# Kernel tuning notes

Hardware: AMD Instinct MI355X
Metric: run time of the kernel (lower is better)

## Reference

```python
import jax, jax.numpy as jnp
import numpy as np

B, C, L, E = 32, 3, 512, 512


def setup_inputs() -> dict:
    key = jax.random.key(0)
    ks = jax.random.split(key, 13)
    bnd = float(np.sqrt(6.0 / (2.0 * E)))  # xavier-uniform-like bound
    uni = lambda k, shp: jax.random.uniform(k, shp, jnp.float32, -bnd, bnd)
    return {
        "A0": jax.random.normal(ks[0], (B, C, L, L), jnp.float32),
        "x0": jax.random.normal(ks[1], (B, C, L, E), jnp.float32),
        "u0": jax.random.normal(ks[2], (B, C, E), jnp.float32),
        "t0": jax.random.normal(ks[3], (B, E), jnp.float32),
        "t1": jax.random.normal(ks[4], (B, E), jnp.float32),
        "Q_weight": uni(ks[5], (C, E, E)),
        "Q_bias": jnp.zeros((C, E), jnp.float32),
        "V_weight": uni(ks[6], (C, E, E)),
        "V_bias": jnp.zeros((C, E), jnp.float32),
        "K_weight": uni(ks[7], (C, E, E)),
        "K_bias": jnp.zeros((C, E), jnp.float32),
        "T_weight": uni(ks[8], (C, E, E)),
        "T_bias": jnp.zeros((C, E), jnp.float32),
    }


def reference(A0, x0, u0, t0, t1,
              Q_weight, Q_bias, V_weight, V_bias,
              K_weight, K_bias, T_weight, T_bias):
    # Time embeddings: (B,E) @ (C,E,E) -> (B,C,E)
    T0 = jnp.einsum('be,cef->bcf', t0, T_weight)
    T1 = jnp.einsum('be,cef->bcf', t1, T_weight)

    # Original modulates weight columns: x @ (W * T) == (x @ W) * T (T broadcasts
    # over the input axis via unsqueeze(-2)); use the fused, equivalent form.
    Q = jnp.einsum('bce,cef->bcf', x0[:, :, -1, :], Q_weight) * T0 + Q_bias  # (B,C,E)
    K = jnp.einsum('bce,cef->bcf', u0, K_weight) * T1 + K_bias               # (B,C,E)
    V = jnp.einsum('bcle,cef->bclf', x0, V_weight) * T1[:, :, None, :] \
        + V_bias[None, :, None, :]                                           # (B,C,L,E)

    QKV = jax.nn.softmax(jnp.einsum('bce,bcle->bcl', Q * K, V), axis=-1)     # (B,C,L)

    # A1[:, :, i, :] = A0[:, :, i+1, :] - A0[:, :, 0, :] for i < L-1;
    # A1[:, :, L-1, :] = A1[:, :, L-2, :] + QKV  (= A0[-1] - A0[0] + QKV)
    rows = A0[:, :, 1:, :] - A0[:, :, :1, :]                                 # (B,C,L-1,L)
    last = rows[:, :, -1, :] + QKV                                           # (B,C,L)
    A1 = jnp.concatenate([rows, last[:, :, None, :]], axis=2)                # (B,C,L,L)

    x1 = jnp.einsum('bclm,bcme->bcle', A1, x0)                               # (B,C,L,E)
    x1 = jnp.diff(x1, axis=2, prepend=jnp.zeros_like(x1[:, :, :1, :]))

    num = jnp.sum(T0 * T1, axis=-1)                                          # (B,C)
    den = jnp.sqrt(jnp.sum(T0 * T0, axis=-1) + jnp.sum(T1 * T1, axis=-1))
    w = (num / den)[..., None]                                               # (B,C,1)

    u1 = u0 * (1.0 - w) + x1.mean(axis=-2) * w                               # (B,C,E)
    return (A1 - A0, x1 - x0, u1 - u0)
```

## Files before the change

kernel.cpp:

```cpp
#include <hip/hip_runtime.h>
#include <stdint.h>

#define BB 32
#define CC 3
#define LL 512
#define EE 512
#define NBC (BB*CC)

#define O2_OFF ((size_t)NBC*LL*LL)
#define O3_OFF (O2_OFF + (size_t)NBC*LL*EE)

#define WSB_QX    0
#define WSB_H     196608
#define WSB_W     442368
#define WSB_ADIFF ((size_t)512*1024)
#define ADIFF_BYTES ((size_t)NBC*LL*LL*2)
#define WSB_X0T   (WSB_ADIFF + ADIFF_BYTES)
#define WS_FAST_NEED (WSB_X0T + ADIFF_BYTES)

#define NEC 16

typedef short bf16x8 __attribute__((ext_vector_type(8)));
typedef float f32x4  __attribute__((ext_vector_type(4)));

__device__ __forceinline__ float wred_sum(float v){
#pragma unroll
  for (int m = 32; m >= 1; m >>= 1) v += __shfl_xor(v, m, 64);
  return v;
}
__device__ __forceinline__ float wred_max(float v){
#pragma unroll
  for (int m = 32; m >= 1; m >>= 1) v = fmaxf(v, __shfl_xor(v, m, 64));
  return v;
}
__device__ __forceinline__ void f4ma(float4& a, float s, const float4& b){
  a.x = fmaf(s, b.x, a.x); a.y = fmaf(s, b.y, a.y);
  a.z = fmaf(s, b.z, a.z); a.w = fmaf(s, b.w, a.w);
}
__device__ __forceinline__ float4 f4sub(const float4& a, const float4& b){
  return make_float4(a.x-b.x, a.y-b.y, a.z-b.z, a.w-b.w);
}
__device__ __forceinline__ unsigned short f2bf(float x){
  unsigned u = __float_as_uint(x);
  return (unsigned short)((u + 0x7FFFu + ((u >> 16) & 1u)) >> 16);
}
__device__ __forceinline__ float bf2f(unsigned short h){
  return __uint_as_float(((unsigned)h) << 16);
}
__device__ __forceinline__ void split1(float v, unsigned short& hi, unsigned short& lo){
  hi = f2bf(v);
  lo = f2bf(v - bf2f(hi));
}

__global__ __launch_bounds__(512) void k0p(
    const float* __restrict__ x0, const float* __restrict__ u0,
    const float* __restrict__ t0, const float* __restrict__ t1,
    const float* __restrict__ Qw, const float* __restrict__ Kw,
    const float* __restrict__ Tw,
    float* __restrict__ P)
{
  const int bg = blockIdx.x;
  const int c  = blockIdx.y;
  const int ec = blockIdx.z;
  const int b0 = bg*4;
  const int e0 = ec*32;
  const int f  = threadIdx.x;
  __shared__ float vb[4][4][32];
  {
    int vec = f >> 7, j = (f >> 5) & 3, e = f & 31;
    int bb = b0 + j;
    float v;
    if      (vec == 0) v = t0[bb*EE + e0 + e];
    else if (vec == 1) v = t1[bb*EE + e0 + e];
    else if (vec == 2) v = x0[((size_t)(bb*CC + c)*LL + (LL-1))*EE + e0 + e];
    else               v = u0[(size_t)(bb*CC + c)*EE + e0 + e];
    vb[vec][j][e] = v;
  }
  __syncthreads();

  const float* twp = Tw + (size_t)c*EE*EE + (size_t)e0*EE + f;
  const float* qwp = Qw + (size_t)c*EE*EE + (size_t)e0*EE + f;
  const float* kwp = Kw + (size_t)c*EE*EE + (size_t)e0*EE + f;
  float aT0[4]={0,0,0,0}, aT1[4]={0,0,0,0}, aQ[4]={0,0,0,0}, aK[4]={0,0,0,0};
#pragma unroll 8
  for (int e = 0; e < 32; ++e) {
    float wt = twp[(size_t)e*EE];
    float wq = qwp[(size_t)e*EE];
    float wk = kwp[(size_t)e*EE];
#pragma unroll
    for (int j = 0; j < 4; ++j) {
      aT0[j] = fmaf(vb[0][j][e], wt, aT0[j]);
      aT1[j] = fmaf(vb[1][j][e], wt, aT1[j]);
      aQ[j]  = fmaf(vb[2][j][e], wq, aQ[j]);
      aK[j]  = fmaf(vb[3][j][e], wk, aK[j]);
    }
  }
#pragma unroll
  for (int j = 0; j < 4; ++j) {
    int cb = c*BB + b0 + j;
    P[(((size_t)0*NEC + ec)*96 + cb)*EE + f] = aT0[j];
    P[(((size_t)1*NEC + ec)*96 + cb)*EE + f] = aT1[j];
    P[(((size_t)2*NEC + ec)*96 + cb)*EE + f] = aQ[j];
    P[(((size_t)3*NEC + ec)*96 + cb)*EE + f] = aK[j];
  }
}

__global__ __launch_bounds__(512) void k0c(
    const float* __restrict__ P,
    const float* __restrict__ Qb, const float* __restrict__ Kb,
    float* __restrict__ gtbuf, float* __restrict__ ws_w)
{
  const int bc = blockIdx.x;
  const int b = bc / CC, c = bc % CC;
  const int cb = c*BB + b;
  const int f = threadIdx.x;
  const int wid = f >> 6, lane = f & 63;
  __shared__ float red[8][3];
  float aT0=0.f, aT1=0.f, aQ=0.f, aK=0.f;
#pragma unroll
  for (int ec = 0; ec < NEC; ++ec) {
    aT0 += P[(((size_t)0*NEC + ec)*96 + cb)*EE + f];
    aT1 += P[(((size_t)1*NEC + ec)*96 + cb)*EE + f];
    aQ  += P[(((size_t)2*NEC + ec)*96 + cb)*EE + f];
    aK  += P[(((size_t)3*NEC + ec)*96 + cb)*EE + f];
  }
  float Qv = aQ*aT0 + Qb[c*EE + f];
  float Kv = aK*aT1 + Kb[c*EE + f];
  gtbuf[(size_t)cb*EE + f] = Qv*Kv*aT1;
  float pn = wred_sum(aT0*aT1);
  float p0 = wred_sum(aT0*aT0);
  float p1 = wred_sum(aT1*aT1);
  if (lane == 0) { red[wid][0]=pn; red[wid][1]=p0; red[wid][2]=p1; }
  __syncthreads();
  if (f == 0) {
    float sn=0.f, s0=0.f, s1=0.f;
    for (int i=0;i<8;++i){ sn+=red[i][0]; s0+=red[i][1]; s1+=red[i][2]; }
    ws_w[bc] = sn / sqrtf(s0 + s1);
  }
}

__global__ __launch_bounds__(256) void k1_h(
    const float* __restrict__ Vw, const float* __restrict__ gtbuf,
    float* __restrict__ ws_h)
{
  const int nt = blockIdx.x;
  const int c  = blockIdx.y;
  const int n0 = nt*128;
  const int t = threadIdx.x, lane = t & 63, w = t >> 6;
  __shared__ __align__(16) char AgtH[32*1024];
  __shared__ __align__(16) char AgtL[32*1024];
  __shared__ __align__(16) char BvH[128*128];
  __shared__ __align__(16) char BvL[128*128];
  {
    int row = t >> 3, sl = t & 7;
    const float* src = gtbuf + ((size_t)(c*BB + row))*EE + sl*64;
#pragma unroll
    for (int c3 = 0; c3 < 8; ++c3) {
      float4 a = *reinterpret_cast<const float4*>(src + c3*8);
      float4 b = *reinterpret_cast<const float4*>(src + c3*8 + 4);
      ushort4 h0,h1,l0,l1;
      split1(a.x,h0.x,l0.x); split1(a.y,h0.y,l0.y); split1(a.z,h0.z,l0.z); split1(a.w,h0.w,l0.w);
      split1(b.x,h1.x,l1.x); split1(b.y,h1.y,l1.y); split1(b.z,h1.z,l1.z); split1(b.w,h1.w,l1.w);
      int off = row*1024 + sl*128 + ((c3 ^ (row & 7)) << 4);
      *reinterpret_cast<ushort4*>(AgtH + off)     = h0;
      *reinterpret_cast<ushort4*>(AgtH + off + 8) = h1;
      *reinterpret_cast<ushort4*>(AgtL + off)     = l0;
      *reinterpret_cast<ushort4*>(AgtL + off + 8) = l1;
    }
  }
  f32x4 acc[2][2];
#pragma unroll
  for (int mi=0; mi<2; ++mi)
#pragma unroll
    for (int ni=0; ni<2; ++ni) acc[mi][ni] = (f32x4){0.f,0.f,0.f,0.f};

  for (int kk = 0; kk < 8; ++kk) {
    __syncthreads();
    {
      int nl = t >> 1, half = t & 1;
      const float* src = Vw + (size_t)c*EE*EE + (size_t)(n0+nl)*EE + kk*64 + half*32;
#pragma unroll
      for (int q = 0; q < 4; ++q) {
        float4 a = *reinterpret_cast<const float4*>(src + q*8);
        float4 b = *reinterpret_cast<const float4*>(src + q*8 + 4);
        int c3 = half*4 + q;
        ushort4 h0,h1,l0,l1;
        split1(a.x,h0.x,l0.x); split1(a.y,h0.y,l0.y); split1(a.z,h0.z,l0.z); split1(a.w,h0.w,l0.w);
        split1(b.x,h1.x,l1.x); split1(b.y,h1.y,l1.y); split1(b.z,h1.z,l1.z); split1(b.w,h1.w,l1.w);
        int off = nl*128 + ((c3 ^ (nl & 7)) << 4);
        *reinterpret_cast<ushort4*>(BvH + off)     = h0;
        *reinterpret_cast<ushort4*>(BvH + off + 8) = h1;
        *reinterpret_cast<ushort4*>(BvL + off)     = l0;
        *reinterpret_cast<ushort4*>(BvL + off + 8) = l1;
      }
    }
    __syncthreads();
    bf16x8 afH[2][2], afL[2][2], bfH[2][2], bfL[2][2];
#pragma unroll
    for (int mi=0; mi<2; ++mi)
#pragma unroll
      for (int ks=0; ks<2; ++ks) {
        int row = mi*16 + (lane & 15);
        int c3 = ks*4 + (lane >> 4);
        int off = row*1024 + kk*128 + ((c3 ^ (row & 7)) << 4);
        afH[mi][ks] = *reinterpret_cast<const bf16x8*>(AgtH + off);
        afL[mi][ks] = *reinterpret_cast<const bf16x8*>(AgtL + off);
      }
#pragma unroll
    for (int ni=0; ni<2; ++ni)
#pragma unroll
      for (int ks=0; ks<2; ++ks) {
        int n = w*32 + ni*16 + (lane & 15);
        int c3 = ks*4 + (lane >> 4);
        int off = n*128 + ((c3 ^ (n & 7)) << 4);
        bfH[ni][ks] = *reinterpret_cast<const bf16x8*>(BvH + off);
        bfL[ni][ks] = *reinterpret_cast<const bf16x8*>(BvL + off);
      }
#pragma unroll
    for (int mi=0; mi<2; ++mi)
#pragma unroll
      for (int ni=0; ni<2; ++ni)
#pragma unroll
        for (int ks=0; ks<2; ++ks) {
          acc[mi][ni] = __builtin_amdgcn_mfma_f32_16x16x32_bf16(afH[mi][ks], bfH[ni][ks], acc[mi][ni], 0, 0, 0);
          acc[mi][ni] = __builtin_amdgcn_mfma_f32_16x16x32_bf16(afH[mi][ks], bfL[ni][ks], acc[mi][ni], 0, 0, 0);
          acc[mi][ni] = __builtin_amdgcn_mfma_f32_16x16x32_bf16(afL[mi][ks], bfH[ni][ks], acc[mi][ni], 0, 0, 0);
        }
  }
#pragma unroll
  for (int mi=0; mi<2; ++mi)
#pragma unroll
    for (int ni=0; ni<2; ++ni)
#pragma unroll
      for (int r=0; r<4; ++r) {
        int b = mi*16 + (lane >> 4)*4 + r;
        int e = n0 + w*32 + ni*16 + (lane & 15);
        ws_h[((size_t)(b*CC + c))*EE + e] = acc[mi][ni][r];
      }
}

__global__ __launch_bounds__(512) void k2a_softmax(
    const float* __restrict__ A0, const float* __restrict__ x0,
    const float* __restrict__ ws_h,
    float* __restrict__ out1)
{
  const int bc = blockIdx.x;
  const int tid = threadIdx.x, wid = tid >> 6, lane = tid & 63;
  __shared__ __align__(16) float hb[EE], sb[LL], a0r0[LL];
  __shared__ float red[8];
  const size_t abase = (size_t)bc*LL*LL;
  const size_t xbase = (size_t)bc*LL*EE;
  hb[tid]   = ws_h[(size_t)bc*EE + tid];
  a0r0[tid] = A0[abase + tid];
  __syncthreads();
  const float4 h0 = *reinterpret_cast<const float4*>(&hb[lane*8]);
  const float4 h1 = *reinterpret_cast<const float4*>(&hb[lane*8+4]);
  for (int l = wid; l < LL; l += 8) {
    const float4* xr = reinterpret_cast<const float4*>(x0 + xbase + (size_t)l*EE);
    float4 v0 = xr[lane*2], v1 = xr[lane*2+1];
    float acc = v0.x*h0.x + v0.y*h0.y + v0.z*h0.z + v0.w*h0.w
              + v1.x*h1.x + v1.y*h1.y + v1.z*h1.z + v1.w*h1.w;
    acc = wred_sum(acc);
    if (lane == 0) sb[l] = acc;
  }
  __syncthreads();
  float v = sb[tid];
  float mx = wred_max(v);
  if (lane == 0) red[wid] = mx;
  __syncthreads();
  mx = red[0];
#pragma unroll
  for (int i = 1; i < 8; ++i) mx = fmaxf(mx, red[i]);
  float ev = __expf(v - mx);
  float sm = wred_sum(ev);
  __syncthreads();
  if (lane == 0) red[wid] = sm;
  __syncthreads();
  float tot = 0.f;
#pragma unroll
  for (int i = 0; i < 8; ++i) tot += red[i];
  float qk = ev / tot;
  out1[abase + (size_t)(LL-1)*LL + tid] = qk - a0r0[tid];
}

__global__ __launch_bounds__(512) void k2b_cols(
    const float* __restrict__ A0, const float* __restrict__ x0,
    const float* __restrict__ u0, const float* __restrict__ out1,
    const float* __restrict__ ws_w,
    float* __restrict__ ws_qx, float* __restrict__ out3)
{
  const int bc = blockIdx.x;
  const int tid = threadIdx.x;
  const size_t abase = (size_t)bc*LL*LL;
  const size_t xbase = (size_t)bc*LL*EE;
  __shared__ __align__(16) float qkv[LL], r0v[LL], r3v[LL];
  __shared__ float partl[4][12][128];
  {
    float a0 = A0[abase + tid];
    float a3 = A0[abase + (size_t)(LL-1)*LL + tid];
    qkv[tid] = out1[abase + (size_t)(LL-1)*LL + tid] + a0;
    r0v[tid] = a0;
    r3v[tid] = a3;
  }
  __syncthreads();
  const int mg = tid >> 7, cg = tid & 127;
  float4 aq = make_float4(0,0,0,0), a0s = make_float4(0,0,0,0), a3s = make_float4(0,0,0,0);
#pragma unroll 4
  for (int i = 0; i < 128; ++i) {
    int m = mg*128 + i;
    float4 xv = *reinterpret_cast<const float4*>(x0 + xbase + (size_t)m*EE + cg*4);
    float qm = qkv[m], z0 = r0v[m], z3 = r3v[m];
    f4ma(aq, qm, xv); f4ma(a0s, z0, xv); f4ma(a3s, z3, xv);
  }
#pragma unroll
  for (int k = 0; k < 4; ++k) {
    partl[mg][0+k][cg] = (&aq.x)[k];
    partl[mg][4+k][cg] = (&a0s.x)[k];
    partl[mg][8+k][cg] = (&a3s.x)[k];
  }
  __syncthreads();
  if (mg == 0) {
    float wv = ws_w[bc];
    float4 uv = *reinterpret_cast<const float4*>(u0 + (size_t)bc*EE + cg*4);
    float4 qx4, o3;
#pragma unroll
    for (int k = 0; k < 4; ++k) {
      float q = 0.f, y0 = 0.f, y3 = 0.f;
#pragma unroll
      for (int g = 0; g < 4; ++g) {
        q  += partl[g][0+k][cg];
        y0 += partl[g][4+k][cg];
        y3 += partl[g][8+k][cg];
      }
      (&qx4.x)[k] = q;
      (&o3.x)[k] = wv * ((y3 - y0 + q) * (1.f/(float)LL) - (&uv.x)[k]);
    }
    *reinterpret_cast<float4*>(ws_qx + (size_t)bc*EE + cg*4) = qx4;
    *reinterpret_cast<float4*>(out3 + (size_t)bc*EE + cg*4) = o3;
  }
}

__global__ __launch_bounds__(512) void k_conv2(
    const float* __restrict__ A0, const float* __restrict__ x0,
    float* __restrict__ out1, char* __restrict__ adiff, char* __restrict__ x0t)
{
  const int bc = blockIdx.x;
  const int tile = blockIdx.y;
  const int t = threadIdx.x;
  if (blockIdx.z == 0) {
    const int r0 = tile*64;
    const size_t abase = (size_t)bc*LL*LL;
    char* ad = adiff + (size_t)bc*LL*LL*2;
    __shared__ __align__(16) float r0f[LL];
    r0f[t] = A0[abase + t];
    __syncthreads();
#pragma unroll 4
    for (int rep = 0; rep < 16; ++rep) {
      int pos = rep*512 + t;
      int rl = pos >> 7;
      int q  = pos & 127;
      int gr = r0 + rl;
      float4 d;
      if (gr < LL-1) {
        float4 a = *reinterpret_cast<const float4*>(A0 + abase + (size_t)gr*LL + q*4);
        float4 b = *reinterpret_cast<const float4*>(A0 + abase + (size_t)(gr+1)*LL + q*4);
        d = make_float4(b.x-a.x, b.y-a.y, b.z-a.z, b.w-a.w);
        float4 z = *reinterpret_cast<const float4*>(&r0f[q*4]);
        *reinterpret_cast<float4*>(out1 + abase + (size_t)gr*LL + q*4) = f4sub(d, z);
      } else {
        d = make_float4(0.f,0.f,0.f,0.f);
      }
      ushort4 pk;
      pk.x = f2bf(d.x); pk.y = f2bf(d.y); pk.z = f2bf(d.z); pk.w = f2bf(d.w);
      *reinterpret_cast<ushort4*>(ad + (size_t)gr*1024 + q*8) = pk;
    }
  } else {
    const int m0 = tile*64;
    const size_t xbase = (size_t)bc*LL*EE;
    char* xt = x0t + (size_t)bc*LL*EE*2;
    __shared__ float T[64][65];
    for (int ech = 0; ech < 8; ++ech) {
      const int e0 = ech*64;
      {
        int ml = t >> 3, seg = t & 7;
        const float* src = x0 + xbase + (size_t)(m0+ml)*EE + e0 + seg*8;
        float4 v0 = *reinterpret_cast<const float4*>(src);
        float4 v1 = *reinterpret_cast<const float4*>(src+4);
        T[ml][seg*8+0]=v0.x; T[ml][seg*8+1]=v0.y; T[ml][seg*8+2]=v0.z; T[ml][seg*8+3]=v0.w;
        T[ml][seg*8+4]=v1.x; T[ml][seg*8+5]=v1.y; T[ml][seg*8+6]=v1.z; T[ml][seg*8+7]=v1.w;
      }
      __syncthreads();
      {
        int el = t >> 3, c3 = t & 7;
        int eg = e0 + el;
        int mb = c3*8;
        ushort4 p0, p1;
        p0.x = f2bf(T[mb+0][el]); p0.y = f2bf(T[mb+1][el]);
        p0.z = f2bf(T[mb+2][el]); p0.w = f2bf(T[mb+3][el]);
        p1.x = f2bf(T[mb+4][el]); p1.y = f2bf(T[mb+5][el]);
        p1.z = f2bf(T[mb+6][el]); p1.w = f2bf(T[mb+7][el]);
        char* dst = xt + (size_t)eg*1024 + (size_t)(m0 + mb)*2;
        *reinterpret_cast<ushort4*>(dst) = p0;
        *reinterpret_cast<ushort4*>(dst + 8) = p1;
      }
      __syncthreads();
    }
  }
}

#define ASTR 80
__global__ __launch_bounds__(256) void k3_bf(
    const char* __restrict__ adiff, const char* __restrict__ x0t,
    const float* __restrict__ x0, const float* __restrict__ ws_qx,
    float* __restrict__ out2)
{
  const int bc = blockIdx.y;
  const int rt = blockIdx.x >> 2, nt = blockIdx.x & 3;
  const int r0 = rt*128, n0b = nt*128;
  const int t = threadIdx.x;
  const int lane = t & 63, wid = t >> 6;
  const int wr = wid >> 1, wc = wid & 1;
  __shared__ __align__(16) char As[128*ASTR];
  __shared__ __align__(16) char Bs[128*ASTR];
  const char* ad = adiff + (size_t)bc*LL*LL*2;
  const char* xt = x0t  + (size_t)bc*LL*EE*2;
  const size_t xbase = (size_t)bc*LL*EE;
  f32x4 acc[4][4];
#pragma unroll
  for (int mi=0; mi<4; ++mi)
#pragma unroll
    for (int ni=0; ni<4; ++ni) acc[mi][ni] = (f32x4){0.f,0.f,0.f,0.f};

  for (int k0 = 0; k0 < LL; k0 += 32) {
    __syncthreads();
#pragma unroll
    for (int i = 0; i < 2; ++i) {
      int idx = i*256 + t;
      int row = idx >> 2, c = idx & 3;
      int4 v = *reinterpret_cast<const int4*>(ad + (size_t)(r0+row)*1024 + k0*2 + c*16);
      *reinterpret_cast<int4*>(As + row*ASTR + c*16) = v;
    }
#pragma unroll
    for (int i = 0; i < 2; ++i) {
      int idx = i*256 + t;
      int n = idx >> 2, c = idx & 3;
      int4 v = *reinterpret_cast<const int4*>(xt + (size_t)(n0b+n)*1024 + k0*2 + c*16);
      int kb = (c*16) ^ (((n >> 2) & 3) << 4);
      *reinterpret_cast<int4*>(Bs + n*ASTR + kb) = v;
    }
    __syncthreads();
    bf16x8 af[4], bfv[4];
#pragma unroll
    for (int mi=0; mi<4; ++mi) {
      int row = wr*64 + mi*16 + (lane & 15);
      af[mi] = *reinterpret_cast<const bf16x8*>(As + row*ASTR + ((lane>>4)*16));
    }
#pragma unroll
    for (int ni=0; ni<4; ++ni) {
      int n = wc*64 + ni*16 + (lane & 15);
      int kb = ((lane>>4)*16) ^ (((n >> 2) & 3) << 4);
      bfv[ni] = *reinterpret_cast<const bf16x8*>(Bs + n*ASTR + kb);
    }
#pragma unroll
    for (int mi=0; mi<4; ++mi)
#pragma unroll
      for (int ni=0; ni<4; ++ni)
        acc[mi][ni] = __builtin_amdgcn_mfma_f32_16x16x32_bf16(af[mi], bfv[ni], acc[mi][ni], 0, 0, 0);
  }
#pragma unroll
  for (int mi=0; mi<4; ++mi)
#pragma unroll
    for (int r=0; r<4; ++r) {
      int grow = r0 + wr*64 + mi*16 + (lane>>4)*4 + r;
      const size_t rowoff = xbase + (size_t)grow*EE;
#pragma unroll
      for (int ni=0; ni<4; ++ni) {
        int gcol = n0b + wc*64 + ni*16 + (lane & 15);
        float xv = x0[rowoff + gcol];
        float val;
        if (grow == LL-1) val = ws_qx[(size_t)bc*EE + gcol] - xv;
        else              val = acc[mi][ni][r] - xv;
        out2[rowoff + gcol] = val;
      }
    }
}

__global__ __launch_bounds__(512) void kA_fused(
    const float* __restrict__ A0, const float* __restrict__ x0,
    const float* __restrict__ u0,
    const float* __restrict__ t0, const float* __restrict__ t1,
    const float* __restrict__ Qw, const float* __restrict__ Qb,
    const float* __restrict__ Vw,
    const float* __restrict__ Kw, const float* __restrict__ Kb,
    const float* __restrict__ Tw,
    float* __restrict__ ws_qx, float* __restrict__ out1, float* __restrict__ out3)
{
  const int bc = blockIdx.x;
  const int b = bc / CC, c = bc % CC;
  const int tid = threadIdx.x;
  const int wid = tid >> 6, lane = tid & 63;
  __shared__ __align__(16) float t0v[EE], t1v[EE], xl[EE], uv[EE], gt[EE];
  __shared__ __align__(16) float hb[EE], sb[LL], a0r0[LL], a0r3[LL];
  __shared__ float red[3][8];
  __shared__ float wsh;
  const size_t abase = (size_t)bc*LL*LL;
  const size_t xbase = (size_t)bc*LL*EE;

  t0v[tid] = t0[b*EE + tid];
  t1v[tid] = t1[b*EE + tid];
  xl[tid]  = x0[xbase + (size_t)(LL-1)*EE + tid];
  uv[tid]  = u0[(size_t)bc*EE + tid];
  a0r0[tid] = A0[abase + tid];
  a0r3[tid] = A0[abase + (size_t)(LL-1)*LL + tid];
  __syncthreads();

  const int f = tid;
  const float* twp = Tw + (size_t)c*EE*EE + f;
  const float* qwp = Qw + (size_t)c*EE*EE + f;
  const float* kwp = Kw + (size_t)c*EE*EE + f;
  float aT0 = 0.f, aT1 = 0.f, aQ = 0.f, aK = 0.f;
  for (int e = 0; e < EE; ++e) {
    float wt = twp[(size_t)e*EE];
    aT0 = fmaf(t0v[e], wt, aT0);
    aT1 = fmaf(t1v[e], wt, aT1);
    aQ  = fmaf(xl[e],  qwp[(size_t)e*EE], aQ);
    aK  = fmaf(uv[e],  kwp[(size_t)e*EE], aK);
  }
  float Qv = aQ*aT0 + Qb[c*EE + f];
  float Kv = aK*aT1 + Kb[c*EE + f];
  gt[f] = Qv*Kv*aT1;

  float pn = wred_sum(aT0*aT1);
  float p0 = wred_sum(aT0*aT0);
  float p1 = wred_sum(aT1*aT1);
  if (lane == 0) { red[0][wid]=pn; red[1][wid]=p0; red[2][wid]=p1; }
  __syncthreads();
  if (tid == 0) {
    float sn=0.f, s0=0.f, s1=0.f;
    for (int i=0;i<8;++i){ sn+=red[0][i]; s0+=red[1][i]; s1+=red[2][i]; }
    wsh = sn / sqrtf(s0 + s1);
  }
  {
    const float4 g0 = *reinterpret_cast<const float4*>(&gt[lane*8]);
    const float4 g1 = *reinterpret_cast<const float4*>(&gt[lane*8+4]);
    for (int r = wid; r < EE; r += 8) {
      const float4* vr = reinterpret_cast<const float4*>(Vw + ((size_t)c*EE + r)*EE);
      float4 v0 = vr[lane*2], v1 = vr[lane*2+1];
      float acc = v0.x*g0.x + v0.y*g0.y + v0.z*g0.z + v0.w*g0.w
                + v1.x*g1.x + v1.y*g1.y + v1.z*g1.z + v1.w*g1.w;
      acc = wred_sum(acc);
      if (lane == 0) hb[r] = acc;
    }
  }
  __syncthreads();

  {
    const float4 h0 = *reinterpret_cast<const float4*>(&hb[lane*8]);
    const float4 h1 = *reinterpret_cast<const float4*>(&hb[lane*8+4]);
    for (int l = wid; l < LL; l += 8) {
      const float4* xr = reinterpret_cast<const float4*>(x0 + xbase + (size_t)l*EE);
      float4 v0 = xr[lane*2], v1 = xr[lane*2+1];
      float acc = v0.x*h0.x + v0.y*h0.y + v0.z*h0.z + v0.w*h0.w
                + v1.x*h1.x + v1.y*h1.y + v1.z*h1.z + v1.w*h1.w;
      acc = wred_sum(acc);
      if (lane == 0) sb[l] = acc;
    }
  }
  __syncthreads();

  float v = sb[tid];
  float mx = wred_max(v);
  if (lane == 0) red[0][wid] = mx;
  __syncthreads();
  mx = red[0][0];
#pragma unroll
  for (int i = 1; i < 8; ++i) mx = fmaxf(mx, red[0][i]);
  float ev = __expf(v - mx);
  float sm = wred_sum(ev);
  __syncthreads();
  if (lane == 0) red[0][wid] = sm;
  __syncthreads();
  float tot = 0.f;
#pragma unroll
  for (int i = 0; i < 8; ++i) tot += red[0][i];
  float qk = ev / tot;
  sb[tid] = qk;
  out1[abase + (size_t)(LL-1)*LL + tid] = qk - a0r0[tid];
  __syncthreads();

  float qx=0.f, y0=0.f, y3=0.f;
  for (int m = 0; m < LL; ++m) {
    float xm = x0[xbase + (size_t)m*EE + tid];
    qx = fmaf(sb[m],   xm, qx);
    y0 = fmaf(a0r0[m], xm, y0);
    y3 = fmaf(a0r3[m], xm, y3);
  }
  ws_qx[(size_t)bc*EE + tid] = qx;
  float mean = (y3 - y0 + qx) * (1.f/(float)LL);
  out3[(size_t)bc*EE + tid] = wsh * (mean - uv[tid]);
}

__global__ __launch_bounds__(256) void k3_mfma(
    const float* __restrict__ A0, const float* __restrict__ x0,
    const float* __restrict__ ws_qx,
    float* __restrict__ out1, float* __restrict__ out2)
{
  const int bc = blockIdx.y;
  const int rt = blockIdx.x >> 2, nt = blockIdx.x & 3;
  const int r0 = rt*128, n0b = nt*128;
  const int t = threadIdx.x;
  const int lane = t & 63, wid = t >> 6;
  const int wr = wid >> 1, wc = wid & 1;
  __shared__ __align__(16) char As[128*ASTR];
  __shared__ __align__(16) char Bs[128*ASTR];
  const size_t abase = (size_t)bc*LL*LL;
  const size_t xbase = (size_t)bc*LL*EE;
  f32x4 acc[4][4];
#pragma unroll
  for (int mi=0; mi<4; ++mi)
#pragma unroll
    for (int ni=0; ni<4; ++ni) acc[mi][ni] = (f32x4){0.f,0.f,0.f,0.f};
  const int bkl = (t & 7) * 4;
  const int bn0 = (t >> 3) * 4;
  for (int k0 = 0; k0 < LL; k0 += 32) {
    __syncthreads();
#pragma unroll
    for (int i = 0; i < 4; ++i) {
      int idx = i*256 + t;
      int row = idx >> 3, kq = idx & 7;
      int gr = r0 + row;
      int gr1 = (gr+1 > LL-1) ? (LL-1) : (gr+1);
      float4 va = *reinterpret_cast<const float4*>(A0 + abase + (size_t)gr *LL + k0 + kq*4);
      float4 vb = *reinterpret_cast<const float4*>(A0 + abase + (size_t)gr1*LL + k0 + kq*4);
      ushort4 pk;
      pk.x = f2bf(vb.x - va.x); pk.y = f2bf(vb.y - va.y);
      pk.z = f2bf(vb.z - va.z); pk.w = f2bf(vb.w - va.w);
      *reinterpret_cast<ushort4*>(As + row*ASTR + kq*8) = pk;
      if (nt == 0 && gr < LL-1) {
        float4 az = *reinterpret_cast<const float4*>(A0 + abase + k0 + kq*4);
        float4 o = make_float4(vb.x - az.x - va.x, vb.y - az.y - va.y,
                               vb.z - az.z - va.z, vb.w - az.w - va.w);
        *reinterpret_cast<float4*>(out1 + abase + (size_t)gr*LL + k0 + kq*4) = o;
      }
    }
    {
      float xq[4][4];
#pragma unroll
      for (int i = 0; i < 4; ++i)
        *reinterpret_cast<float4*>(xq[i]) =
          *reinterpret_cast<const float4*>(x0 + xbase + (size_t)(k0+bkl+i)*EE + n0b + bn0);
#pragma unroll
      for (int j = 0; j < 4; ++j) {
        int n = bn0 + j;
        ushort4 pk;
        pk.x = f2bf(xq[0][j]); pk.y = f2bf(xq[1][j]);
        pk.z = f2bf(xq[2][j]); pk.w = f2bf(xq[3][j]);
        int kb = (bkl*2) ^ (((n >> 2) & 3) << 4);
        *reinterpret_cast<ushort4*>(Bs + n*ASTR + kb) = pk;
      }
    }
    __syncthreads();
    bf16x8 af[4], bfv[4];
#pragma unroll
    for (int mi=0; mi<4; ++mi) {
      int row = wr*64 + mi*16 + (lane & 15);
      af[mi] = *reinterpret_cast<const bf16x8*>(As + row*ASTR + ((lane>>4)*16));
    }
#pragma unroll
    for (int ni=0; ni<4; ++ni) {
      int n = wc*64 + ni*16 + (lane & 15);
      int kb = ((lane>>4)*16) ^ (((n >> 2) & 3) << 4);
      bfv[ni] = *reinterpret_cast<const bf16x8*>(Bs + n*ASTR + kb);
    }
#pragma unroll
    for (int mi=0; mi<4; ++mi)
#pragma unroll
      for (int ni=0; ni<4; ++ni)
        acc[mi][ni] = __builtin_amdgcn_mfma_f32_16x16x32_bf16(af[mi], bfv[ni], acc[mi][ni], 0, 0, 0);
  }
#pragma unroll
  for (int mi=0; mi<4; ++mi)
#pragma unroll
    for (int r=0; r<4; ++r) {
      int grow = r0 + wr*64 + mi*16 + (lane>>4)*4 + r;
      const size_t rowoff = xbase + (size_t)grow*EE;
#pragma unroll
      for (int ni=0; ni<4; ++ni) {
        int gcol = n0b + wc*64 + ni*16 + (lane & 15);
        float xv = x0[rowoff + gcol];
        float val;
        if (grow == LL-1) val = ws_qx[(size_t)bc*EE + gcol] - xv;
        else              val = acc[mi][ni][r] - xv;
        out2[rowoff + gcol] = val;
      }
    }
}

extern "C" void kernel_launch(void* const* d_in, const int* in_sizes, int n_in,
                              void* d_out, int out_size, void* d_ws, size_t ws_size,
                              hipStream_t stream)
{
  const float* A0 = (const float*)d_in[0];
  const float* x0 = (const float*)d_in[1];
  const float* u0 = (const float*)d_in[2];
  const float* t0 = (const float*)d_in[3];
  const float* t1 = (const float*)d_in[4];
  const float* Qw = (const float*)d_in[5];
  const float* Qb = (const float*)d_in[6];
  const float* Vw = (const float*)d_in[7];
  const float* Kw = (const float*)d_in[9];
  const float* Kb = (const float*)d_in[10];
  const float* Tw = (const float*)d_in[11];

  char*  wsb    = (char*)d_ws;
  float* ws_qx  = (float*)(wsb + WSB_QX);
  float* ws_h   = (float*)(wsb + WSB_H);
  float* ws_w   = (float*)(wsb + WSB_W);

  float* out1 = (float*)d_out;
  float* out2 = out1 + O2_OFF;
  float* out3 = out1 + O3_OFF;
  float* gtbuf = out3;
  float* pscr  = out2;

  const bool fast = ws_size >= WS_FAST_NEED;

  if (fast) {
    char* adiff = wsb + WSB_ADIFF;
    char* x0t   = wsb + WSB_X0T;
    k_conv2<<<dim3(NBC, 8, 2), 512, 0, stream>>>(A0, x0, out1, adiff, x0t);
    k0p<<<dim3(8, 3, NEC), 512, 0, stream>>>(x0, u0, t0, t1, Qw, Kw, Tw, pscr);
    k0c<<<NBC, 512, 0, stream>>>(pscr, Qb, Kb, gtbuf, ws_w);
    k1_h<<<dim3(4, 3), 256, 0, stream>>>(Vw, gtbuf, ws_h);
    k2a_softmax<<<NBC, 512, 0, stream>>>(A0, x0, ws_h, out1);
    k2b_cols<<<NBC, 512, 0, stream>>>(A0, x0, u0, out1, ws_w, ws_qx, out3);
    k3_bf<<<dim3(16, NBC), 256, 0, stream>>>(adiff, x0t, x0, ws_qx, out2);
  } else {
    kA_fused<<<NBC, 512, 0, stream>>>(A0, x0, u0, t0, t1, Qw, Qb, Vw, Kw, Kb, Tw,
                                      ws_qx, out1, out3);
    k3_mfma<<<dim3(16, NBC), 256, 0, stream>>>(A0, x0, ws_qx, out1, out2);
  }
}
```

Before: 272.1 us.

## Drop x0 transpose pre-pass; convert x0 to bf16 in GEMM loader, fuse softmax+cols

```diff
diff --git a/kernel.cpp b/kernel.cpp
--- a/kernel.cpp
+++ b/kernel.cpp
@@ -15,8 +15,7 @@
 #define WSB_W     442368
 #define WSB_ADIFF ((size_t)512*1024)
 #define ADIFF_BYTES ((size_t)NBC*LL*LL*2)
-#define WSB_X0T   (WSB_ADIFF + ADIFF_BYTES)
-#define WS_FAST_NEED (WSB_X0T + ADIFF_BYTES)
+#define WS_FAST_NEED (WSB_ADIFF + ADIFF_BYTES)
 
 #define NEC 16
 
@@ -239,19 +238,22 @@
       }
 }
 
-__global__ __launch_bounds__(512) void k2a_softmax(
+__global__ __launch_bounds__(512) void k2f(
     const float* __restrict__ A0, const float* __restrict__ x0,
-    const float* __restrict__ ws_h,
-    float* __restrict__ out1)
+    const float* __restrict__ u0,
+    const float* __restrict__ ws_h, const float* __restrict__ ws_w,
+    float* __restrict__ ws_qx, float* __restrict__ out1, float* __restrict__ out3)
 {
   const int bc = blockIdx.x;
   const int tid = threadIdx.x, wid = tid >> 6, lane = tid & 63;
-  __shared__ __align__(16) float hb[EE], sb[LL], a0r0[LL];
+  __shared__ __align__(16) float hb[EE], sb[LL], a0r0[LL], a0r3[LL];
   __shared__ float red[8];
+  __shared__ float partl[4][12][128];
   const size_t abase = (size_t)bc*LL*LL;
   const size_t xbase = (size_t)bc*LL*EE;
   hb[tid]   = ws_h[(size_t)bc*EE + tid];
   a0r0[tid] = A0[abase + tid];
+  a0r3[tid] = A0[abase + (size_t)(LL-1)*LL + tid];
   __syncthreads();
   const float4 h0 = *reinterpret_cast<const float4*>(&hb[lane*8]);
   const float4 h1 = *reinterpret_cast<const float4*>(&hb[lane*8+4]);
@@ -280,28 +282,8 @@
 #pragma unroll
   for (int i = 0; i < 8; ++i) tot += red[i];
   float qk = ev / tot;
+  sb[tid] = qk;
   out1[abase + (size_t)(LL-1)*LL + tid] = qk - a0r0[tid];
-}
-
-__global__ __launch_bounds__(512) void k2b_cols(
-    const float* __restrict__ A0, const float* __restrict__ x0,
-    const float* __restrict__ u0, const float* __restrict__ out1,
-    const float* __restrict__ ws_w,
-    float* __restrict__ ws_qx, float* __restrict__ out3)
-{
-  const int bc = blockIdx.x;
-  const int tid = threadIdx.x;
-  const size_t abase = (size_t)bc*LL*LL;
-  const size_t xbase = (size_t)bc*LL*EE;
-  __shared__ __align__(16) float qkv[LL], r0v[LL], r3v[LL];
-  __shared__ float partl[4][12][128];
-  {
-    float a0 = A0[abase + tid];
-    float a3 = A0[abase + (size_t)(LL-1)*LL + tid];
-    qkv[tid] = out1[abase + (size_t)(LL-1)*LL + tid] + a0;
-    r0v[tid] = a0;
-    r3v[tid] = a3;
-  }
   __syncthreads();
   const int mg = tid >> 7, cg = tid & 127;
   float4 aq = make_float4(0,0,0,0), a0s = make_float4(0,0,0,0), a3s = make_float4(0,0,0,0);
@@ -309,7 +291,7 @@
   for (int i = 0; i < 128; ++i) {
     int m = mg*128 + i;
     float4 xv = *reinterpret_cast<const float4*>(x0 + xbase + (size_t)m*EE + cg*4);
-    float qm = qkv[m], z0 = r0v[m], z3 = r3v[m];
+    float qm = sb[m], z0 = a0r0[m], z3 = a0r3[m];
     f4ma(aq, qm, xv); f4ma(a0s, z0, xv); f4ma(a3s, z3, xv);
   }
 #pragma unroll
@@ -340,79 +322,44 @@
   }
 }
 
-__global__ __launch_bounds__(512) void k_conv2(
-    const float* __restrict__ A0, const float* __restrict__ x0,
-    float* __restrict__ out1, char* __restrict__ adiff, char* __restrict__ x0t)
+__global__ __launch_bounds__(512) void k_conv3(
+    const float* __restrict__ A0, float* __restrict__ out1, char* __restrict__ adiff)
 {
   const int bc = blockIdx.x;
   const int tile = blockIdx.y;
   const int t = threadIdx.x;
-  if (blockIdx.z == 0) {
-    const int r0 = tile*64;
-    const size_t abase = (size_t)bc*LL*LL;
-    char* ad = adiff + (size_t)bc*LL*LL*2;
-    __shared__ __align__(16) float r0f[LL];
-    r0f[t] = A0[abase + t];
-    __syncthreads();
+  const int r0 = tile*64;
+  const size_t abase = (size_t)bc*LL*LL;
+  char* ad = adiff + (size_t)bc*LL*LL*2;
+  __shared__ __align__(16) float r0f[LL];
+  r0f[t] = A0[abase + t];
+  __syncthreads();
 #pragma unroll 4
-    for (int rep = 0; rep < 16; ++rep) {
-      int pos = rep*512 + t;
-      int rl = pos >> 7;
-      int q  = pos & 127;
-      int gr = r0 + rl;
-      float4 d;
-      if (gr < LL-1) {
-        float4 a = *reinterpret_cast<const float4*>(A0 + abase + (size_t)gr*LL + q*4);
-        float4 b = *reinterpret_cast<const float4*>(A0 + abase + (size_t)(gr+1)*LL + q*4);
-        d = make_float4(b.x-a.x, b.y-a.y, b.z-a.z, b.w-a.w);
-        float4 z = *reinterpret_cast<const float4*>(&r0f[q*4]);
-        *reinterpret_cast<float4*>(out1 + abase + (size_t)gr*LL + q*4) = f4sub(d, z);
-      } else {
-        d = make_float4(0.f,0.f,0.f,0.f);
-      }
-      ushort4 pk;
-      pk.x = f2bf(d.x); pk.y = f2bf(d.y); pk.z = f2bf(d.z); pk.w = f2bf(d.w);
-      *reinterpret_cast<ushort4*>(ad + (size_t)gr*1024 + q*8) = pk;
-    }
-  } else {
-    const int m0 = tile*64;
-    const size_t xbase = (size_t)bc*LL*EE;
-    char* xt = x0t + (size_t)bc*LL*EE*2;
-    __shared__ float T[64][65];
-    for (int ech = 0; ech < 8; ++ech) {
-      const int e0 = ech*64;
-      {
-        int ml = t >> 3, seg = t & 7;
-        const float* src = x0 + xbase + (size_t)(m0+ml)*EE + e0 + seg*8;
-        float4 v0 = *reinterpret_cast<const float4*>(src);
-        float4 v1 = *reinterpret_cast<const float4*>(src+4);
-        T[ml][seg*8+0]=v0.x; T[ml][seg*8+1]=v0.y; T[ml][seg*8+2]=v0.z; T[ml][seg*8+3]=v0.w;
-        T[ml][seg*8+4]=v1.x; T[ml][seg*8+5]=v1.y; T[ml][seg*8+6]=v1.z; T[ml][seg*8+7]=v1.w;
-      }
-      __syncthreads();
-      {
-        int el = t >> 3, c3 = t & 7;
-        int eg = e0 + el;
-        int mb = c3*8;
-        ushort4 p0, p1;
-        p0.x = f2bf(T[mb+0][el]); p0.y = f2bf(T[mb+1][el]);
-        p0.z = f2bf(T[mb+2][el]); p0.w = f2bf(T[mb+3][el]);
-        p1.x = f2bf(T[mb+4][el]); p1.y = f2bf(T[mb+5][el]);
-        p1.z = f2bf(T[mb+6][el]); p1.w = f2bf(T[mb+7][el]);
-        char* dst = xt + (size_t)eg*1024 + (size_t)(m0 + mb)*2;
-        *reinterpret_cast<ushort4*>(dst) = p0;
-        *reinterpret_cast<ushort4*>(dst + 8) = p1;
-      }
-      __syncthreads();
-    }
+  for (int rep = 0; rep < 16; ++rep) {
+    int pos = rep*512 + t;
+    int rl = pos >> 7;
+    int q  = pos & 127;
+    int gr = r0 + rl;
+    float4 d;
+    if (gr < LL-1) {
+      float4 a = *reinterpret_cast<const float4*>(A0 + abase + (size_t)gr*LL + q*4);
+      float4 b = *reinterpret_cast<const float4*>(A0 + abase + (size_t)(gr+1)*LL + q*4);
+      d = make_float4(b.x-a.x, b.y-a.y, b.z-a.z, b.w-a.w);
+      float4 z = *reinterpret_cast<const float4*>(&r0f[q*4]);
+      *reinterpret_cast<float4*>(out1 + abase + (size_t)gr*LL + q*4) = f4sub(d, z);
+    } else {
+      d = make_float4(0.f,0.f,0.f,0.f);
+    }
+    ushort4 pk;
+    pk.x = f2bf(d.x); pk.y = f2bf(d.y); pk.z = f2bf(d.z); pk.w = f2bf(d.w);
+    *reinterpret_cast<ushort4*>(ad + (size_t)gr*1024 + q*8) = pk;
   }
 }
 
 #define ASTR 80
-__global__ __launch_bounds__(256) void k3_bf(
-    const char* __restrict__ adiff, const char* __restrict__ x0t,
-    const float* __restrict__ x0, const float* __restrict__ ws_qx,
-    float* __restrict__ out2)
+__global__ __launch_bounds__(256) void k3_bf2(
+    const char* __restrict__ adiff, const float* __restrict__ x0,
+    const float* __restrict__ ws_qx, float* __restrict__ out2)
 {
   const int bc = blockIdx.y;
   const int rt = blockIdx.x >> 2, nt = blockIdx.x & 3;
@@ -423,13 +370,15 @@
   __shared__ __align__(16) char As[128*ASTR];
   __shared__ __align__(16) char Bs[128*ASTR];
   const char* ad = adiff + (size_t)bc*LL*LL*2;
-  const char* xt = x0t  + (size_t)bc*LL*EE*2;
   const size_t xbase = (size_t)bc*LL*EE;
   f32x4 acc[4][4];
 #pragma unroll
   for (int mi=0; mi<4; ++mi)
 #pragma unroll
     for (int ni=0; ni<4; ++ni) acc[mi][ni] = (f32x4){0.f,0.f,0.f,0.f};
+
+  const int bkl = (t & 7) * 4;
+  const int bn0 = (t >> 3) * 4;
 
   for (int k0 = 0; k0 < LL; k0 += 32) {
     __syncthreads();
@@ -440,13 +389,21 @@
       int4 v = *reinterpret_cast<const int4*>(ad + (size_t)(r0+row)*1024 + k0*2 + c*16);
       *reinterpret_cast<int4*>(As + row*ASTR + c*16) = v;
     }
-#pragma unroll
-    for (int i = 0; i < 2; ++i) {
-      int idx = i*256 + t;
-      int n = idx >> 2, c = idx & 3;
-      int4 v = *reinterpret_cast<const int4*>(xt + (size_t)(n0b+n)*1024 + k0*2 + c*16);
-      int kb = (c*16) ^ (((n >> 2) & 3) << 4);
-      *reinterpret_cast<int4*>(Bs + n*ASTR + kb) = v;
+    {
+      float xq[4][4];
+#pragma unroll
+      for (int i = 0; i < 4; ++i)
+        *reinterpret_cast<float4*>(xq[i]) =
+          *reinterpret_cast<const float4*>(x0 + xbase + (size_t)(k0+bkl+i)*EE + n0b + bn0);
+#pragma unroll
+      for (int j = 0; j < 4; ++j) {
+        int n = bn0 + j;
+        ushort4 pk;
+        pk.x = f2bf(xq[0][j]); pk.y = f2bf(xq[1][j]);
+        pk.z = f2bf(xq[2][j]); pk.w = f2bf(xq[3][j]);
+        int kb = (bkl*2) ^ (((n >> 2) & 3) << 4);
+        *reinterpret_cast<ushort4*>(Bs + n*ASTR + kb) = pk;
+      }
     }
     __syncthreads();
     bf16x8 af[4], bfv[4];
@@ -727,14 +684,12 @@
 
   if (fast) {
     char* adiff = wsb + WSB_ADIFF;
-    char* x0t   = wsb + WSB_X0T;
-    k_conv2<<<dim3(NBC, 8, 2), 512, 0, stream>>>(A0, x0, out1, adiff, x0t);
+    k_conv3<<<dim3(NBC, 8), 512, 0, stream>>>(A0, out1, adiff);
     k0p<<<dim3(8, 3, NEC), 512, 0, stream>>>(x0, u0, t0, t1, Qw, Kw, Tw, pscr);
     k0c<<<NBC, 512, 0, stream>>>(pscr, Qb, Kb, gtbuf, ws_w);
     k1_h<<<dim3(4, 3), 256, 0, stream>>>(Vw, gtbuf, ws_h);
-    k2a_softmax<<<NBC, 512, 0, stream>>>(A0, x0, ws_h, out1);
-    k2b_cols<<<NBC, 512, 0, stream>>>(A0, x0, u0, out1, ws_w, ws_qx, out3);
-    k3_bf<<<dim3(16, NBC), 256, 0, stream>>>(adiff, x0t, x0, ws_qx, out2);
+    k2f<<<NBC, 512, 0, stream>>>(A0, x0, u0, ws_h, ws_w, ws_qx, out1, out3);
+    k3_bf2<<<dim3(16, NBC), 256, 0, stream>>>(adiff, x0, ws_qx, out2);
   } else {
     kA_fused<<<NBC, 512, 0, stream>>>(A0, x0, u0, t0, t1, Qw, Qb, Vw, Kw, Kb, Tw,
                                       ws_qx, out1, out3);
```

Result: no change. 269.4 us (-1.0%).
